# Kernel tuning notes

Hardware: AMD Instinct MI355X
Metric: run time of the kernel (lower is better)

The kernel has to match this reference:

```python
import jax, jax.numpy as jnp
import numpy as np

D_MODEL = 1024

def setup_inputs() -> dict:
    key = jax.random.key(0)
    k1, k2 = jax.random.split(key, 2)
    x = jax.random.normal(k1, (4, 2048, D_MODEL), dtype=jnp.float32)
    W_attn = jax.random.normal(k2, (3 * D_MODEL, D_MODEL), dtype=jnp.float32) * (1.0 / np.sqrt(D_MODEL))
    b_attn = jnp.zeros((3 * D_MODEL,), dtype=jnp.float32)
    return {"x": x, "W_attn": W_attn, "b_attn": b_attn}

def reference(x, W_attn, b_attn):
    B, T, C = x.shape
    # fused QKV projection; torch split order is (k, q, v)
    kqv = x @ W_attn.T + b_attn            # [B, T, 3C]
    k, q, v = jnp.split(kqv, 3, axis=-1)   # each [B, T, C]
    # NOTE: original computes k @ q^T (quirk), scaled by sqrt(d_model)
    scores = jnp.einsum('btc,bsc->bts', k, q) / jnp.sqrt(jnp.asarray(C, x.dtype))
    causal = jnp.tril(jnp.ones((T, T), dtype=bool))
    scores = jnp.where(causal[None, :, :], scores, -jnp.inf)
    attn = jax.nn.softmax(scores, axis=-1)
    return jnp.einsum('bts,bsc->btc', attn, v)
```

## Files before the change

### kernel.cpp

```cpp
#include <hip/hip_runtime.h>

typedef __bf16 bf16x8 __attribute__((ext_vector_type(8)));
typedef float f32x4 __attribute__((ext_vector_type(4)));
typedef float fl4 __attribute__((ext_vector_type(4)));
typedef unsigned short us4 __attribute__((ext_vector_type(4)));
typedef unsigned short us8 __attribute__((ext_vector_type(8)));

__device__ __forceinline__ unsigned short f2bf(float f) {
  unsigned u = __builtin_bit_cast(unsigned, f);
  u += 0x7fffu + ((u >> 16) & 1u);
  return (unsigned short)(u >> 16);
}
__device__ __forceinline__ float bf2f(unsigned short h) {
  unsigned u = ((unsigned)h) << 16;
  return __builtin_bit_cast(float, u);
}

__device__ __forceinline__ void async16(const void* g, void* l) {
  __builtin_amdgcn_global_load_lds(
      (const __attribute__((address_space(1))) unsigned int*)g,
      (__attribute__((address_space(3))) unsigned int*)l, 16, 0, 0);
}

#define BARM() asm volatile("s_barrier" ::: "memory")
#define VMCNT4() asm volatile("s_waitcnt vmcnt(4)" ::: "memory")
#define VMCNT6() asm volatile("s_waitcnt vmcnt(6)" ::: "memory")
#define LGKM0() asm volatile("s_waitcnt lgkmcnt(0)" ::: "memory")
#define LGKM8() asm volatile("s_waitcnt lgkmcnt(8)" ::: "memory")
#define SCHEDB() __builtin_amdgcn_sched_barrier(0)

__global__ __launch_bounds__(256) void cvt_bf16_2(const float* __restrict__ sA,
                                                  unsigned short* __restrict__ dA, int nA,
                                                  const float* __restrict__ sB,
                                                  unsigned short* __restrict__ dB, int nB) {
  int i = blockIdx.x * 256 + threadIdx.x;
  const float* s;
  unsigned short* d;
  if (i < nA) {
    s = sA; d = dA;
  } else {
    i -= nA;
    if (i >= nB) return;
    s = sB; d = dB;
  }
  fl4 f = ((const fl4*)s)[i];
  us4 o;
  o[0] = f2bf(f[0]); o[1] = f2bf(f[1]); o[2] = f2bf(f[2]); o[3] = f2bf(f[3]);
  ((us4*)d)[i] = o;
}

__global__ __launch_bounds__(256) void transpose_v(const unsigned short* __restrict__ kqv,
                                                   unsigned short* __restrict__ vT) {
  int b = blockIdx.z;
  int t0 = blockIdx.x * 64;
  int c0 = blockIdx.y * 64;
  __shared__ unsigned short tile[64][68];
  int tid = threadIdx.x;
#pragma unroll
  for (int i = 0; i < 4; ++i) {
    int idx = i * 256 + tid;
    int r = idx >> 4;
    int c4 = (idx & 15) * 4;
    const unsigned short* src = kqv + ((size_t)(b * 2048 + t0 + r)) * 3072 + 2048 + c0 + c4;
    us4 v = *(const us4*)src;
    *(us4*)&tile[r][c4] = v;
  }
  __syncthreads();
#pragma unroll
  for (int i = 0; i < 4; ++i) {
    int idx = i * 256 + tid;
    int rc = idx >> 4;
    int t4 = (idx & 15) * 4;
    us4 v;
    v[0] = tile[t4 + 0][rc]; v[1] = tile[t4 + 1][rc];
    v[2] = tile[t4 + 2][rc]; v[3] = tile[t4 + 3][rc];
    unsigned short* dst = vT + ((size_t)(b * 1024 + c0 + rc)) * 2048 + t0 + t4;
    *(us4*)dst = v;
  }
}

__global__ __launch_bounds__(512, 2) void gemm_g0(
    const unsigned short* __restrict__ A, const unsigned short* __restrict__ B,
    unsigned short* __restrict__ C, const float* __restrict__ bias) {
  const int flat = blockIdx.x;
  const int swz = (flat & 7) * 64 + (flat >> 3);
  const int bx = swz & 7;
  const int by = swz >> 3;
  const int rowBase = by * 128, colBase = bx * 384;
  const int lda = 1024, ldc = 3072, nk = 16;

  __shared__ __align__(16) unsigned char lds[131072];
  const int tid = threadIdx.x;
  const int lane = tid & 63, wid = tid >> 6;
  const int wr = wid >> 2, wc = wid & 3;
  const int l15 = lane & 15, l4 = lane >> 4, l7 = lane & 7;

  f32x4 acc[4][6] = {};
  bf16x8 af01[2][2], af23[2][2], bf[6][2];

  const unsigned short* Ab = A + (size_t)rowBase * lda;
  const unsigned short* Bb = B + (size_t)colBase * lda;
  unsigned aoff[2], boff[6], aldso[2], bldso[6];
#pragma unroll
  for (int i = 0; i < 6; ++i) {
    int off = i * 8192 + tid * 16;
    int r = off >> 7;
    int sb = ((off >> 4) & 7) ^ (r & 7);
    if (i < 2) { aoff[i] = (unsigned)(r * lda + sb * 8); aldso[i] = (unsigned)off; }
    boff[i] = (unsigned)(r * lda + sb * 8);
    bldso[i] = (unsigned)off;
  }

  auto STA = [&](int bufc, int op, int koff) {
    async16(Ab + (size_t)(aoff[op] + (unsigned)koff), lds + bufc * 65536 + aldso[op]);
  };
  auto STB = [&](int bufc, int op, int koff) {
    async16(Bb + (size_t)(boff[op] + (unsigned)koff),
            lds + bufc * 65536 + 16384 + bldso[op]);
  };
  auto RA = [&](int bufc, int m, int kk) -> bf16x8 {
    int row = wr * 64 + m * 16 + l15;
    int blk = (kk * 4 + l4) ^ l7;
    return *(const bf16x8*)(lds + bufc * 65536 + row * 128 + blk * 16);
  };
  auto RB = [&](int bufc, int n, int kk) -> bf16x8 {
    int row = wc * 96 + n * 16 + l15;
    int blk = (kk * 4 + l4) ^ l7;
    return *(const bf16x8*)(lds + bufc * 65536 + 16384 + row * 128 + blk * 16);
  };

#define RD_A01(BUF)                                                            \
  _Pragma("unroll") for (int mi = 0; mi < 2; ++mi)                             \
  _Pragma("unroll") for (int kk = 0; kk < 2; ++kk) af01[mi][kk] = RA((BUF), mi, kk)
#define RD_A23(BUF)                                                            \
  _Pragma("unroll") for (int mi = 0; mi < 2; ++mi)                             \
  _Pragma("unroll") for (int kk = 0; kk < 2; ++kk) af23[mi][kk] = RA((BUF), 2 + mi, kk)
#define RD_B(BUF, N0)                                                          \
  _Pragma("unroll") for (int nj = 0; nj < 3; ++nj)                             \
  _Pragma("unroll") for (int kk = 0; kk < 2; ++kk) bf[(N0) + nj][kk] = RB((BUF), (N0) + nj, kk)

#define MQ(MB, NB, AF)                                                         \
  _Pragma("unroll") for (int kk = 0; kk < 2; ++kk)                             \
  _Pragma("unroll") for (int mi = 0; mi < 2; ++mi)                             \
  _Pragma("unroll") for (int nj = 0; nj < 3; ++nj)                             \
      acc[(MB) + mi][(NB) + nj] = __builtin_amdgcn_mfma_f32_16x16x32_bf16(     \
          AF[mi][kk], bf[(NB) + nj][kk], acc[(MB) + mi][(NB) + nj], 0, 0, 0)

#define PHASE(RDS, STG, GATE, MB, NB, AF)                                      \
  do {                                                                         \
    RDS;                                                                       \
    STG;                                                                       \
    BARM();                                                                    \
    LGKM0();                                                                   \
    SCHEDB();                                                                  \
    __builtin_amdgcn_s_setprio(1);                                             \
    MQ(MB, NB, AF);                                                            \
    __builtin_amdgcn_s_setprio(0);                                             \
    GATE;                                                                      \
    BARM();                                                                    \
  } while (0)

  STA(0, 0, 0); STA(0, 1, 0);
#pragma unroll
  for (int i = 0; i < 6; ++i) STB(0, i, 0);
#pragma unroll
  for (int i = 0; i < 6; ++i) STB(1, i, 64);
  VMCNT6();
  BARM();

  for (int it = 0; it < 8; ++it) {
    int t = it * 2;
    int kA1 = (t + 1) * 64;
    int k2 = (t + 2 < nk - 1 ? t + 2 : nk - 1) * 64;
    int k3 = (t + 3 < nk - 1 ? t + 3 : nk - 1) * 64;
    PHASE({ RD_A01(0); RD_B(0, 0); }, { STA(1, 0, kA1); STA(1, 1, kA1); },
          (void)0, 0, 0, af01);
    PHASE({ RD_A23(0); RD_B(0, 3); }, (void)0, (void)0, 0, 3, af01);
    PHASE({}, { STB(0, 0, k2); STB(0, 1, k2); STB(0, 2, k2); },
          (void)0, 2, 3, af23);
    PHASE({}, { STB(0, 3, k2); STB(0, 4, k2); STB(0, 5, k2); },
          VMCNT6(), 2, 0, af23);
    PHASE({ RD_A01(1); RD_B(1, 0); }, { STA(0, 0, k2); STA(0, 1, k2); },
          (void)0, 0, 0, af01);
    PHASE({ RD_A23(1); RD_B(1, 3); }, (void)0, (void)0, 0, 3, af01);
    PHASE({}, { STB(1, 0, k3); STB(1, 1, k3); STB(1, 2, k3); },
          (void)0, 2, 3, af23);
    PHASE({}, { STB(1, 3, k3); STB(1, 4, k3); STB(1, 5, k3); },
          VMCNT6(), 2, 0, af23);
  }
#undef PHASE
#undef MQ
#undef RD_A01
#undef RD_A23
#undef RD_B

  const int cr = l4 * 4;
#pragma unroll
  for (int n = 0; n < 6; ++n) {
    int col = colBase + wc * 96 + n * 16 + l15;
    float bv = bias[col];
#pragma unroll
    for (int m = 0; m < 4; ++m) {
      int row = rowBase + wr * 64 + m * 16 + cr;
#pragma unroll
      for (int i = 0; i < 4; ++i)
        C[(size_t)(row + i) * ldc + col] = f2bf(acc[m][n][i] + bv);
    }
  }
}

template <int EPI>
__global__ __launch_bounds__(512, 2) void gemm8p(
    const unsigned short* __restrict__ A, int lda, long long sA,
    const unsigned short* __restrict__ B, int ldb, long long sB,
    void* __restrict__ Cv, int ldc, long long sC,
    float scale, int K) {
  int bx = blockIdx.x, by = blockIdx.y;
  const int bz = blockIdx.z;
  if (EPI == 1 && bx > by) return;
  A += (size_t)bz * sA;
  B += (size_t)bz * sB;
  const int rowBase = by * 256;
  const int colBase = bx * 256;
  const int nk = (EPI == 2) ? (rowBase + 256) / 64 : K / 64;

  __shared__ __align__(16) unsigned char lds[131072];
  const int tid = threadIdx.x;
  const int lane = tid & 63;
  const int wid = tid >> 6;
  const int wr = wid >> 2;
  const int wc = wid & 3;
  const int l15 = lane & 15, l4 = lane >> 4, l7 = lane & 7;

  f32x4 acc[8][4] = {};
  bf16x8 af0[4][2], af1[4][2], bf0[2][2], bf1[2][2];

  const unsigned short* Ab = A + (size_t)rowBase * lda;
  const unsigned short* Bb = B + (size_t)colBase * ldb;
  unsigned loff[2][2];
  unsigned lldso[2];
#pragma unroll
  for (int i = 0; i < 2; ++i) {
    int off = (i * 512 + tid) * 16;
    int r = off >> 7;
    int sb = ((off >> 4) & 7) ^ (r & 7);
    lldso[i] = (unsigned)off;
#pragma unroll
    for (int h = 0; h < 2; ++h)
      loff[h][i] = (unsigned)((h * 128 + r) * lda + sb * 8);
  }

  auto STAGE = [&](int bufc, int isB, int half, const unsigned short* Gb, int koff) {
#pragma unroll
    for (int i = 0; i < 2; ++i)
      async16(Gb + (size_t)(loff[half][i] + (unsigned)koff),
              lds + bufc * 65536 + isB * 32768 + half * 16384 + lldso[i]);
  };
  auto RDA = [&](int bufc, int m, int kk) -> bf16x8 {
    int row = m * 16 + l15;
    int blk = (kk * 4 + l4) ^ l7;
    return *(const bf16x8*)(lds + bufc * 65536 + wr * 16384 + row * 128 + blk * 16);
  };
  auto RDB = [&](int bufc, int n, int kk) -> bf16x8 {
    int row = (wc & 1) * 64 + n * 16 + l15;
    int blk = (kk * 4 + l4) ^ l7;
    return *(const bf16x8*)(lds + bufc * 65536 + 32768 + (wc >> 1) * 16384 +
                            row * 128 + blk * 16);
  };

#define RDA8(dst, BUF, Q)                                                      \
  _Pragma("unroll") for (int mi = 0; mi < 4; ++mi)                             \
  _Pragma("unroll") for (int kk = 0; kk < 2; ++kk)                             \
      dst[mi][kk] = RDA((BUF), (Q) * 4 + mi, kk)
#define RDB4(dst, BUF, NB)                                                     \
  _Pragma("unroll") for (int nj = 0; nj < 2; ++nj)                             \
  _Pragma("unroll") for (int kk = 0; kk < 2; ++kk)                             \
      dst[nj][kk] = RDB((BUF), (NB) + nj, kk)

#define MFMAQ(MB, NB, AF, BF)                                                  \
  _Pragma("unroll") for (int kk = 0; kk < 2; ++kk)                             \
  _Pragma("unroll") for (int mi = 0; mi < 4; ++mi)                             \
  _Pragma("unroll") for (int nj = 0; nj < 2; ++nj)                             \
      acc[(MB) + mi][(NB) + nj] = __builtin_amdgcn_mfma_f32_16x16x32_bf16(     \
          AF[mi][kk], BF[nj][kk], acc[(MB) + mi][(NB) + nj], 0, 0, 0)

#define PH(RDS, STG, HINT, GATE, MB, NB, AF, BF)                               \
  do {                                                                         \
    RDS;                                                                       \
    STG;                                                                       \
    HINT;                                                                      \
    BARM();                                                                    \
    LGKM0();                                                                   \
    SCHEDB();                                                                  \
    __builtin_amdgcn_s_setprio(1);                                             \
    MFMAQ(MB, NB, AF, BF);                                                     \
    __builtin_amdgcn_s_setprio(0);                                             \
    GATE;                                                                      \
    BARM();                                                                    \
  } while (0)

  STAGE(0, 0, 0, Ab, 0);
  STAGE(0, 0, 1, Ab, 0);
  STAGE(0, 1, 0, Bb, 0);
  STAGE(0, 1, 1, Bb, 0);
  {
    int k1 = ((1 < nk - 1) ? 1 : (nk - 1)) * 64;
    STAGE(1, 1, 0, Bb, k1);
    STAGE(1, 1, 1, Bb, k1);
  }
  VMCNT4();
  BARM();

  const int nt2 = nk >> 1;
  for (int it = 0; it < nt2; ++it) {
    int t = it * 2;
    int kA1 = (t + 1) * 64;
    int k2 = (t + 2 < nk - 1 ? t + 2 : nk - 1) * 64;
    int k3 = (t + 3 < nk - 1 ? t + 3 : nk - 1) * 64;
    PH({ RDA8(af0, 0, 0); RDB4(bf0, 0, 0); }, STAGE(1, 0, 0, Ab, kA1), LGKM8(),
       (void)0, 0, 0, af0, bf0);
    PH({ RDB4(bf1, 0, 2); }, STAGE(1, 0, 1, Ab, kA1), (void)0,
       (void)0, 0, 2, af0, bf1);
    PH({ RDA8(af1, 0, 1); }, STAGE(0, 1, 0, Bb, k2), (void)0,
       (void)0, 4, 2, af1, bf1);
    PH({}, STAGE(0, 1, 1, Bb, k2), (void)0,
       VMCNT4(), 4, 0, af1, bf0);
    PH({ RDA8(af0, 1, 0); RDB4(bf0, 1, 0); }, STAGE(0, 0, 0, Ab, k2), LGKM8(),
       (void)0, 0, 0, af0, bf0);
    PH({ RDB4(bf1, 1, 2); }, STAGE(0, 0, 1, Ab, k2), (void)0,
       (void)0, 0, 2, af0, bf1);
    PH({ RDA8(af1, 1, 1); }, STAGE(1, 1, 0, Bb, k3), (void)0,
       (void)0, 4, 2, af1, bf1);
    PH({}, STAGE(1, 1, 1, Bb, k3), (void)0,
       VMCNT4(), 4, 0, af1, bf0);
  }
#undef PH
#undef MFMAQ
#undef RDA8
#undef RDB4

  const int cr = l4 * 4;
  if constexpr (EPI == 1) {
    unsigned short* C = (unsigned short*)Cv + (size_t)bz * sC;
#pragma unroll
    for (int n = 0; n < 4; ++n) {
      int col = colBase + wc * 64 + n * 16 + l15;
#pragma unroll
      for (int m = 0; m < 8; ++m) {
        int row = rowBase + wr * 128 + m * 16 + cr;
#pragma unroll
        for (int i = 0; i < 4; ++i)
          C[(size_t)(row + i) * ldc + col] = f2bf(acc[m][n][i] * scale);
      }
    }
  } else {
    float* C = (float*)Cv + (size_t)bz * sC;
#pragma unroll
    for (int n = 0; n < 4; ++n) {
      int col = colBase + wc * 64 + n * 16 + l15;
#pragma unroll
      for (int m = 0; m < 8; ++m) {
        int row = rowBase + wr * 128 + m * 16 + cr;
#pragma unroll
        for (int i = 0; i < 4; ++i)
          C[(size_t)(row + i) * ldc + col] = acc[m][n][i];
      }
    }
  }
}

__global__ __launch_bounds__(256) void softmax_causal(unsigned short* __restrict__ S) {
  const int T = 2048;
  int t = blockIdx.x, b = blockIdx.y;
  unsigned short* row = S + ((size_t)b * T + t) * T;
  const int nv = t + 1;
  const int bound = ((t >> 8) + 1) << 8;
  int tid = threadIdx.x;
  int lane = tid & 63, wid = tid >> 6;
  int s0 = tid * 8;
  us8 raw = {};
  if (s0 < nv) raw = *(const us8*)(row + s0);
  float v[8];
  float m = -3.0e38f;
#pragma unroll
  for (int j = 0; j < 8; ++j) {
    v[j] = bf2f(raw[j]);
    if (s0 + j < nv) m = fmaxf(m, v[j]);
  }
#pragma unroll
  for (int o = 32; o > 0; o >>= 1) m = fmaxf(m, __shfl_xor(m, o, 64));
  __shared__ float red[4];
  if (lane == 0) red[wid] = m;
  __syncthreads();
  m = fmaxf(fmaxf(red[0], red[1]), fmaxf(red[2], red[3]));
  __syncthreads();
  float sum = 0.f;
#pragma unroll
  for (int j = 0; j < 8; ++j) {
    float e = (s0 + j < nv) ? exp2f(v[j] - m) : 0.f;
    v[j] = e;
    sum += e;
  }
#pragma unroll
  for (int o = 32; o > 0; o >>= 1) sum += __shfl_xor(sum, o, 64);
  if (lane == 0) red[wid] = sum;
  __syncthreads();
  sum = red[0] + red[1] + red[2] + red[3];
  float inv = 1.0f / sum;
  if (s0 < bound) {
    us8 outv;
#pragma unroll
    for (int j = 0; j < 8; ++j) outv[j] = f2bf(v[j] * inv);
    *(us8*)(row + s0) = outv;
  }
}

extern "C" void kernel_launch(void* const* d_in, const int* in_sizes, int n_in,
                              void* d_out, int out_size, void* d_ws, size_t ws_size,
                              hipStream_t stream) {
  const float* x = (const float*)d_in[0];
  const float* W = (const float*)d_in[1];
  const float* bias = (const float*)d_in[2];
  float* out = (float*)d_out;

  char* ws = (char*)d_ws;
  if (ws_size < 106954752u) return;
  unsigned short* xbf = (unsigned short*)(ws);
  unsigned short* vT = xbf;
  unsigned short* wbf = (unsigned short*)(ws + 16777216);
  unsigned short* kqv = (unsigned short*)(ws + 23068672);
  unsigned short* S = (unsigned short*)(ws + 73400320);

  const float kSoftmaxScale = 1.4426950408889634f / 32.0f;

  cvt_bf16_2<<<11264, 256, 0, stream>>>(x, xbf, 2097152, W, wbf, 786432);

  gemm_g0<<<dim3(512, 1, 1), 512, 0, stream>>>(xbf, wbf, kqv, bias);

  transpose_v<<<dim3(32, 16, 4), 256, 0, stream>>>(kqv, vT);

  gemm8p<1><<<dim3(8, 8, 4), 512, 0, stream>>>(
      kqv, 3072, 2048LL * 3072, kqv + 1024, 3072, 2048LL * 3072,
      S, 2048, 2048LL * 2048, kSoftmaxScale, 1024);

  softmax_causal<<<dim3(2048, 4), 256, 0, stream>>>(S);

  gemm8p<2><<<dim3(4, 8, 4), 512, 0, stream>>>(
      S, 2048, 2048LL * 2048, vT, 2048, 1024LL * 2048,
      out, 1024, 2048LL * 1024, 1.0f, 2048);
}
```

Before: 184.6 us.

## Split-K the causal PV GEMM across two halves with atomic accumulation

The attention-times-V GEMM now splits each row block's causal K range into two halves, each run by its own workgroup, doubling the grid. Results are combined with float atomic adds into an output zeroed by a memset up front. Heavy row blocks are also scheduled first to reduce tail imbalance. This raises parallelism on a grid that was small and triangular-imbalanced, at the cost of an extra memset, atomic traffic and nondeterministic summation order.

```diff
diff --git a/kernel.cpp b/kernel.cpp
--- a/kernel.cpp
+++ b/kernel.cpp
@@ -215,14 +215,23 @@
     const unsigned short* __restrict__ B, int ldb, long long sB,
     void* __restrict__ Cv, int ldc, long long sC,
     float scale, int K) {
-  int bx = blockIdx.x, by = blockIdx.y;
+  int bx = blockIdx.x, by = blockIdx.y, h = 0;
   const int bz = blockIdx.z;
   if (EPI == 1 && bx > by) return;
+  if (EPI == 2) { by = 7 - (blockIdx.y >> 1); h = blockIdx.y & 1; }
   A += (size_t)bz * sA;
   B += (size_t)bz * sB;
   const int rowBase = by * 256;
   const int colBase = bx * 256;
-  const int nk = (EPI == 2) ? (rowBase + 256) / 64 : K / 64;
+  int kt0, nkh;
+  if (EPI == 2) {
+    int nk = (rowBase + 256) / 64;
+    nkh = nk >> 1;
+    kt0 = h * nkh;
+  } else {
+    kt0 = 0; nkh = K / 64;
+  }
+  const int ktEnd = kt0 + nkh - 1;
 
   __shared__ __align__(16) unsigned char lds[131072];
   const int tid = threadIdx.x;
@@ -246,8 +255,8 @@
     int sb = ((off >> 4) & 7) ^ (r & 7);
     lldso[i] = (unsigned)off;
 #pragma unroll
-    for (int h = 0; h < 2; ++h)
-      loff[h][i] = (unsigned)((h * 128 + r) * lda + sb * 8);
+    for (int hh = 0; hh < 2; ++hh)
+      loff[hh][i] = (unsigned)((hh * 128 + r) * lda + sb * 8);
   }
 
   auto STAGE = [&](int bufc, int isB, int half, const unsigned short* Gb, int koff) {
@@ -299,24 +308,24 @@
     BARM();                                                                    \
   } while (0)
 
-  STAGE(0, 0, 0, Ab, 0);
-  STAGE(0, 0, 1, Ab, 0);
-  STAGE(0, 1, 0, Bb, 0);
-  STAGE(0, 1, 1, Bb, 0);
+  STAGE(0, 0, 0, Ab, kt0 * 64);
+  STAGE(0, 0, 1, Ab, kt0 * 64);
+  STAGE(0, 1, 0, Bb, kt0 * 64);
+  STAGE(0, 1, 1, Bb, kt0 * 64);
   {
-    int k1 = ((1 < nk - 1) ? 1 : (nk - 1)) * 64;
+    int k1 = ((kt0 + 1 < ktEnd) ? kt0 + 1 : ktEnd) * 64;
     STAGE(1, 1, 0, Bb, k1);
     STAGE(1, 1, 1, Bb, k1);
   }
   VMCNT4();
   BARM();
 
-  const int nt2 = nk >> 1;
+  const int nt2 = nkh >> 1;
   for (int it = 0; it < nt2; ++it) {
-    int t = it * 2;
+    int t = kt0 + it * 2;
     int kA1 = (t + 1) * 64;
-    int k2 = (t + 2 < nk - 1 ? t + 2 : nk - 1) * 64;
-    int k3 = (t + 3 < nk - 1 ? t + 3 : nk - 1) * 64;
+    int k2 = (t + 2 < ktEnd ? t + 2 : ktEnd) * 64;
+    int k3 = (t + 3 < ktEnd ? t + 3 : ktEnd) * 64;
     PH({ RDA8(af0, 0, 0); RDB4(bf0, 0, 0); }, STAGE(1, 0, 0, Ab, kA1), LGKM8(),
        (void)0, 0, 0, af0, bf0);
     PH({ RDB4(bf1, 0, 2); }, STAGE(1, 0, 1, Ab, kA1), (void)0,
@@ -363,7 +372,7 @@
         int row = rowBase + wr * 128 + m * 16 + cr;
 #pragma unroll
         for (int i = 0; i < 4; ++i)
-          C[(size_t)(row + i) * ldc + col] = acc[m][n][i];
+          unsafeAtomicAdd(&C[(size_t)(row + i) * ldc + col], acc[m][n][i]);
       }
     }
   }
@@ -433,6 +442,8 @@
 
   const float kSoftmaxScale = 1.4426950408889634f / 32.0f;
 
+  hipMemsetAsync(out, 0, (size_t)out_size * 4, stream);
+
   cvt_bf16_2<<<11264, 256, 0, stream>>>(x, xbf, 2097152, W, wbf, 786432);
 
   gemm_g0<<<dim3(512, 1, 1), 512, 0, stream>>>(xbf, wbf, kqv, bias);
@@ -445,7 +456,7 @@
 
   softmax_causal<<<dim3(2048, 4), 256, 0, stream>>>(S);
 
-  gemm8p<2><<<dim3(4, 8, 4), 512, 0, stream>>>(
+  gemm8p<2><<<dim3(4, 16, 4), 512, 0, stream>>>(
       S, 2048, 2048LL * 2048, vT, 2048, 1024LL * 2048,
       out, 1024, 2048LL * 1024, 1.0f, 2048);
 }
```

New measurement: 200.4 us. +8.6%, slower.

## Replace PV GEMM with 128x128 causal-aware kernel and finer softmax bound

Applied to the files above, without the earlier changes.

The P·V product moves from the 256x256 pipelined gemm8p kernel to a new simpler 128x128-tile kernel. Its K loop stops at the causal diagonal in 128-row granularity and row blocks are launched in reverse order so the longest blocks start first. The softmax zero-fill bound is tightened from 256 to 128 columns to match. This cuts wasted work on masked regions and improves load balance, but the new kernel is single-buffered with barriers around every tile, so it loses the copy/compute overlap of the old kernel.

```diff
diff --git a/kernel.cpp b/kernel.cpp
--- a/kernel.cpp
+++ b/kernel.cpp
@@ -209,20 +209,19 @@
   }
 }
 
-template <int EPI>
-__global__ __launch_bounds__(512, 2) void gemm8p(
+__global__ __launch_bounds__(512, 2) void gemm_s(
     const unsigned short* __restrict__ A, int lda, long long sA,
     const unsigned short* __restrict__ B, int ldb, long long sB,
-    void* __restrict__ Cv, int ldc, long long sC,
+    unsigned short* __restrict__ C, int ldc, long long sC,
     float scale, int K) {
   int bx = blockIdx.x, by = blockIdx.y;
   const int bz = blockIdx.z;
-  if (EPI == 1 && bx > by) return;
+  if (bx > by) return;
   A += (size_t)bz * sA;
   B += (size_t)bz * sB;
   const int rowBase = by * 256;
   const int colBase = bx * 256;
-  const int nk = (EPI == 2) ? (rowBase + 256) / 64 : K / 64;
+  const int nk = K / 64;
 
   __shared__ __align__(16) unsigned char lds[131072];
   const int tid = threadIdx.x;
@@ -246,8 +245,8 @@
     int sb = ((off >> 4) & 7) ^ (r & 7);
     lldso[i] = (unsigned)off;
 #pragma unroll
-    for (int h = 0; h < 2; ++h)
-      loff[h][i] = (unsigned)((h * 128 + r) * lda + sb * 8);
+    for (int hh = 0; hh < 2; ++hh)
+      loff[hh][i] = (unsigned)((hh * 128 + r) * lda + sb * 8);
   }
 
   auto STAGE = [&](int bufc, int isB, int half, const unsigned short* Gb, int koff) {
@@ -303,11 +302,8 @@
   STAGE(0, 0, 1, Ab, 0);
   STAGE(0, 1, 0, Bb, 0);
   STAGE(0, 1, 1, Bb, 0);
-  {
-    int k1 = ((1 < nk - 1) ? 1 : (nk - 1)) * 64;
-    STAGE(1, 1, 0, Bb, k1);
-    STAGE(1, 1, 1, Bb, k1);
-  }
+  STAGE(1, 1, 0, Bb, 64);
+  STAGE(1, 1, 1, Bb, 64);
   VMCNT4();
   BARM();
 
@@ -340,31 +336,93 @@
 #undef RDB4
 
   const int cr = l4 * 4;
-  if constexpr (EPI == 1) {
-    unsigned short* C = (unsigned short*)Cv + (size_t)bz * sC;
+  unsigned short* Cb = C + (size_t)bz * sC;
+#pragma unroll
+  for (int n = 0; n < 4; ++n) {
+    int col = colBase + wc * 64 + n * 16 + l15;
+#pragma unroll
+    for (int m = 0; m < 8; ++m) {
+      int row = rowBase + wr * 128 + m * 16 + cr;
+#pragma unroll
+      for (int i = 0; i < 4; ++i)
+        Cb[(size_t)(row + i) * ldc + col] = f2bf(acc[m][n][i] * scale);
+    }
+  }
+}
+
+__global__ __launch_bounds__(256, 2) void gemm_pv(
+    const unsigned short* __restrict__ S, const unsigned short* __restrict__ V,
+    float* __restrict__ O) {
+  const int bx = blockIdx.x;
+  const int by = 15 - (int)blockIdx.y;
+  const int bz = blockIdx.z;
+  const unsigned short* A = S + (size_t)bz * 2048 * 2048 + (size_t)(by * 128) * 2048;
+  const unsigned short* B = V + (size_t)bz * 1024 * 2048 + (size_t)(bx * 128) * 2048;
+  float* Ob = O + (size_t)bz * 2048 * 1024;
+  const int nk = (by + 1) * 2;
+
+  __shared__ __align__(16) unsigned char lds[32768];
+  const int tid = threadIdx.x;
+  const int lane = tid & 63, wid = tid >> 6;
+  const int wr = (wid >> 1) * 64, wc = (wid & 1) * 64;
+  const int l15 = lane & 15, l4 = lane >> 4, l7 = lane & 7;
+
+  f32x4 acc[4][4] = {};
+
+  unsigned goff[4], ldso[4];
+#pragma unroll
+  for (int i = 0; i < 4; ++i) {
+    int off = (i * 256 + tid) * 16;
+    int r = off >> 7;
+    int sb = ((off >> 4) & 7) ^ (r & 7);
+    goff[i] = (unsigned)(r * 2048 + sb * 8);
+    ldso[i] = (unsigned)off;
+  }
+
+  for (int kt = 0; kt < nk; ++kt) {
+    const unsigned kof = (unsigned)(kt * 64);
+    __syncthreads();
+#pragma unroll
+    for (int i = 0; i < 4; ++i) {
+      async16(A + (size_t)(goff[i] + kof), lds + ldso[i]);
+      async16(B + (size_t)(goff[i] + kof), lds + 16384 + ldso[i]);
+    }
+    __syncthreads();
+    bf16x8 af[4][2], bfr[4][2];
+#pragma unroll
+    for (int m = 0; m < 4; ++m) {
+      int row = wr + m * 16 + l15;
+#pragma unroll
+      for (int kk = 0; kk < 2; ++kk)
+        af[m][kk] = *(const bf16x8*)(lds + row * 128 + (((kk * 4 + l4) ^ l7) * 16));
+    }
 #pragma unroll
     for (int n = 0; n < 4; ++n) {
-      int col = colBase + wc * 64 + n * 16 + l15;
-#pragma unroll
-      for (int m = 0; m < 8; ++m) {
-        int row = rowBase + wr * 128 + m * 16 + cr;
-#pragma unroll
-        for (int i = 0; i < 4; ++i)
-          C[(size_t)(row + i) * ldc + col] = f2bf(acc[m][n][i] * scale);
-      }
+      int row = wc + n * 16 + l15;
+#pragma unroll
+      for (int kk = 0; kk < 2; ++kk)
+        bfr[n][kk] = *(const bf16x8*)(lds + 16384 + row * 128 + (((kk * 4 + l4) ^ l7) * 16));
     }
-  } else {
-    float* C = (float*)Cv + (size_t)bz * sC;
-#pragma unroll
-    for (int n = 0; n < 4; ++n) {
-      int col = colBase + wc * 64 + n * 16 + l15;
-#pragma unroll
-      for (int m = 0; m < 8; ++m) {
-        int row = rowBase + wr * 128 + m * 16 + cr;
-#pragma unroll
-        for (int i = 0; i < 4; ++i)
-          C[(size_t)(row + i) * ldc + col] = acc[m][n][i];
-      }
+#pragma unroll
+    for (int kk = 0; kk < 2; ++kk)
+#pragma unroll
+      for (int m = 0; m < 4; ++m)
+#pragma unroll
+        for (int n = 0; n < 4; ++n)
+          acc[m][n] = __builtin_amdgcn_mfma_f32_16x16x32_bf16(af[m][kk], bfr[n][kk],
+                                                              acc[m][n], 0, 0, 0);
+  }
+
+  const int cr = l4 * 4;
+#pragma unroll
+  for (int n = 0; n < 4; ++n) {
+    int col = bx * 128 + wc + n * 16 + l15;
+#pragma unroll
+    for (int m = 0; m < 4; ++m) {
+      int row = by * 128 + wr + m * 16 + cr;
+#pragma unroll
+      for (int i = 0; i < 4; ++i)
+        Ob[(size_t)(row + i) * 1024 + col] = acc[m][n][i];
     }
   }
 }
@@ -374,7 +432,7 @@
   int t = blockIdx.x, b = blockIdx.y;
   unsigned short* row = S + ((size_t)b * T + t) * T;
   const int nv = t + 1;
-  const int bound = ((t >> 8) + 1) << 8;
+  const int bound = ((t >> 7) + 1) << 7;
   int tid = threadIdx.x;
   int lane = tid & 63, wid = tid >> 6;
   int s0 = tid * 8;
@@ -439,13 +497,11 @@
 
   transpose_v<<<dim3(32, 16, 4), 256, 0, stream>>>(kqv, vT);
 
-  gemm8p<1><<<dim3(8, 8, 4), 512, 0, stream>>>(
+  gemm_s<<<dim3(8, 8, 4), 512, 0, stream>>>(
       kqv, 3072, 2048LL * 3072, kqv + 1024, 3072, 2048LL * 3072,
       S, 2048, 2048LL * 2048, kSoftmaxScale, 1024);
 
   softmax_causal<<<dim3(2048, 4), 256, 0, stream>>>(S);
 
-  gemm8p<2><<<dim3(4, 8, 4), 512, 0, stream>>>(
-      S, 2048, 2048LL * 2048, vT, 2048, 1024LL * 2048,
-      out, 1024, 2048LL * 1024, 1.0f, 2048);
-}
+  gemm_pv<<<dim3(8, 16, 4), 256, 0, stream>>>(S, vT, out);
+}
```

Result: faster. 171.3 us (-7.2%).
